# Kernel optimization log

Measured on AMD Instinct MI355X. Metric: run time of the kernel, lower is better.

## Reference

```python
import jax, jax.numpy as jnp
import numpy as np

NEG_SLOPE = 0.01  # nn.LeakyReLU default


def gcn_conv(x, src, dst, deg_inv_sqrt, W, b, n_nodes):
    """PyG GCNConv with self-loops already folded into (src, dst, deg_inv_sqrt).
    out = scatter_add(norm_e * (x @ W)[src]) + b, norm_e = d_src^-1/2 * d_dst^-1/2."""
    h = x @ W  # [N, F_out] -- transform first (F_out < F_in saves gather traffic)
    norm = (deg_inv_sqrt[src] * deg_inv_sqrt[dst])[:, None]  # [E, 1]
    msg = h[src] * norm  # [E, F_out]
    return jax.ops.segment_sum(msg, dst, num_segments=n_nodes) + b


def setup_inputs() -> dict:
    key = jax.random.key(0)
    ks = jax.random.split(key, 8)
    N, E, F_IN, F_HID, F_OUT = 50000, 800000, 256, 128, 64
    x = jax.random.normal(ks[0], (N, F_IN), dtype=jnp.float32)
    edge_index = jax.random.randint(ks[1], (2, E), 0, N, dtype=jnp.int64)
    def glorot(k, shape):
        lim = float(np.sqrt(6.0 / (shape[0] + shape[1])))
        return jax.random.uniform(k, shape, jnp.float32, -lim, lim)
    return {
        "x": x,
        "edge_index": edge_index,
        "W1": glorot(ks[2], (F_IN, F_HID)),
        "b1": jnp.zeros((F_HID,), jnp.float32),
        "W_mu": glorot(ks[3], (F_HID, F_OUT)),
        "b_mu": jnp.zeros((F_OUT,), jnp.float32),
        "W_logvar": glorot(ks[4], (F_HID, F_OUT)),
        "b_logvar": jnp.zeros((F_OUT,), jnp.float32),
    }


def reference(x, edge_index, W1, b1, W_mu, b_mu, W_logvar, b_logvar):
    n_nodes = x.shape[0]
    loops = jnp.arange(n_nodes, dtype=edge_index.dtype)
    src = jnp.concatenate([edge_index[0], loops])
    dst = jnp.concatenate([edge_index[1], loops])
    # degree on destination nodes (includes self-loop); >= 1 so rsqrt is safe
    deg = jax.ops.segment_sum(jnp.ones_like(dst, dtype=x.dtype), dst, num_segments=n_nodes)
    deg_inv_sqrt = jax.lax.rsqrt(deg)

    h = gcn_conv(x, src, dst, deg_inv_sqrt, W1, b1, n_nodes)
    h = jax.nn.leaky_relu(h, NEG_SLOPE)
    mu = gcn_conv(h, src, dst, deg_inv_sqrt, W_mu, b_mu, n_nodes)
    logvar = gcn_conv(h, src, dst, deg_inv_sqrt, W_logvar, b_logvar, n_nodes)
    return (mu, logvar)
```

## Files before the change

kernel.cpp:

```cpp
#include <hip/hip_runtime.h>

#define NEG_SLOPE 0.01f
#define EPB 4096
#define NB_SHIFT 8

typedef __attribute__((ext_vector_type(8))) short bf16x8;
typedef __attribute__((ext_vector_type(4))) float floatx4;

__device__ __forceinline__ short f2bf(float f) {
    union { float f; unsigned u; } v; v.f = f;
    unsigned u = v.u;
    u += 0x7FFF + ((u >> 16) & 1);
    return (short)(u >> 16);
}
__device__ __forceinline__ float bf2f(short s) {
    union { unsigned u; float f; } v;
    v.u = ((unsigned)(unsigned short)s) << 16;
    return v.f;
}

__launch_bounds__(256)
__global__ void hist_pack(const int* __restrict__ dst, int E, int B, int K,
                          int* __restrict__ btot,
                          const float* __restrict__ W1, const float* __restrict__ Wmu,
                          const float* __restrict__ Wlv,
                          short* __restrict__ w1f, short* __restrict__ wcatf) {
    __shared__ int lh[256];
    int bid = blockIdx.x;
    int tid = threadIdx.x;
    if (bid < B) {
        lh[tid] = 0;
        __syncthreads();
        int lo = bid * EPB, hi = min(lo + EPB, E);
        for (int e = lo + tid; e < hi; e += 256)
            atomicAdd(&lh[dst[e] >> NB_SHIFT], 1);
        __syncthreads();
        int v = lh[tid];
        if (v) atomicAdd(&btot[tid], v);
    } else {
        int i = (bid - B) * 256 + tid;
        if (i < 128 * 256) {
            int j  = i & 7;
            int ln = (i >> 3) & 15;
            int q  = (i >> 7) & 3;
            int t  = (i >> 9) & 7;
            int kb = i >> 12;
            int n = t * 16 + ln;
            int k = kb * 32 + q * 8 + j;
            w1f[i] = f2bf(W1[k * 128 + n]);
        } else {
            int i2 = i - 128 * 256;
            int j  = i2 & 7;
            int ln = (i2 >> 3) & 15;
            int q  = (i2 >> 7) & 3;
            int t  = (i2 >> 9) & 7;
            int kb = i2 >> 12;
            int n = t * 16 + ln;
            int k = kb * 32 + q * 8 + j;
            wcatf[i2] = f2bf((n < 64) ? Wmu[k * 64 + n] : Wlv[k * 64 + (n - 64)]);
        }
    }
}

__global__ void bucket_scan(const int* __restrict__ btot, int K, int E,
                            int* __restrict__ bstart, int* __restrict__ bcur) {
    __shared__ int waveTot[4];
    __shared__ int waveOff[4];
    int tid = threadIdx.x;
    int lane = tid & 63, wave = tid >> 6;
    int v = (tid < K) ? btot[tid] : 0;
    int s = v;
    #pragma unroll
    for (int o = 1; o < 64; o <<= 1) {
        int t = __shfl_up(s, o);
        if (lane >= o) s += t;
    }
    if (lane == 63) waveTot[wave] = s;
    __syncthreads();
    if (tid == 0) {
        int acc = 0;
        #pragma unroll
        for (int w = 0; w < 4; w++) { waveOff[w] = acc; acc += waveTot[w]; }
    }
    __syncthreads();
    int excl = s - v + waveOff[wave];
    if (tid < K) { bstart[tid] = excl; bcur[tid] = excl; }
    if (tid == 0) bstart[K] = E;
}

template<int K>
__device__ __forceinline__ void gemm1_body(int blk, int tid, const float* __restrict__ Ap,
                                           const short* __restrict__ Bfrag,
                                           short* __restrict__ C, int M) {
    int w = tid >> 6;
    int lane = tid & 63;
    int ln = lane & 15;
    int q  = lane >> 4;
    int rowTile = blk * 128 + w * 32;

    int r0 = rowTile + ln;
    int r1 = rowTile + 16 + ln;
    int r0c = (r0 < M) ? r0 : (M - 1);
    int r1c = (r1 < M) ? r1 : (M - 1);

    const float* a0F = Ap + (size_t)r0c * K + q * 8;
    const float* a1F = Ap + (size_t)r1c * K + q * 8;
    const short* bLane = Bfrag + lane * 8;

    floatx4 acc[2][8];
    #pragma unroll
    for (int f = 0; f < 2; f++)
        #pragma unroll
        for (int t = 0; t < 8; t++) acc[f][t] = (floatx4){0.f, 0.f, 0.f, 0.f};

    constexpr int NIT = K / 32;
    #pragma unroll
    for (int kb = 0; kb < NIT; kb++) {
        int kt = kb * 32;
        bf16x8 aF0, aF1;
        float4 x0 = *(const float4*)(a0F + kt);
        float4 x1 = *(const float4*)(a0F + kt + 4);
        float4 y0 = *(const float4*)(a1F + kt);
        float4 y1 = *(const float4*)(a1F + kt + 4);
        aF0[0] = f2bf(x0.x); aF0[1] = f2bf(x0.y); aF0[2] = f2bf(x0.z); aF0[3] = f2bf(x0.w);
        aF0[4] = f2bf(x1.x); aF0[5] = f2bf(x1.y); aF0[6] = f2bf(x1.z); aF0[7] = f2bf(x1.w);
        aF1[0] = f2bf(y0.x); aF1[1] = f2bf(y0.y); aF1[2] = f2bf(y0.z); aF1[3] = f2bf(y0.w);
        aF1[4] = f2bf(y1.x); aF1[5] = f2bf(y1.y); aF1[6] = f2bf(y1.z); aF1[7] = f2bf(y1.w);
        bf16x8 bF[8];
        #pragma unroll
        for (int t = 0; t < 8; t++)
            bF[t] = *(const bf16x8*)(bLane + (size_t)(kb * 8 + t) * 512);
        #pragma unroll
        for (int t = 0; t < 8; t++) {
            acc[0][t] = __builtin_amdgcn_mfma_f32_16x16x32_bf16(aF0, bF[t], acc[0][t], 0, 0, 0);
            acc[1][t] = __builtin_amdgcn_mfma_f32_16x16x32_bf16(aF1, bF[t], acc[1][t], 0, 0, 0);
        }
    }

    #pragma unroll
    for (int f = 0; f < 2; f++) {
        #pragma unroll
        for (int reg = 0; reg < 4; reg++) {
            int r = rowTile + f * 16 + q * 4 + reg;
            if (r < M) {
                #pragma unroll
                for (int t = 0; t < 8; t++)
                    C[(size_t)r * 128 + t * 16 + ln] = f2bf(acc[f][t][reg]);
            }
        }
    }
}

__launch_bounds__(256)
__global__ void scatter_gemm1(const int* __restrict__ src, const int* __restrict__ dst,
                              int E, int B, int* __restrict__ bcur,
                              unsigned* __restrict__ bucketed,
                              const float* __restrict__ x, const short* __restrict__ w1f,
                              short* __restrict__ z1, int M) {
    __shared__ int lh[256];
    __shared__ int lofs[256];
    __shared__ int gbase[256];
    __shared__ unsigned srt[EPB];
    __shared__ int waveTot[4];
    __shared__ int waveOff[4];
    int bid = blockIdx.x;
    int tid = threadIdx.x;
    if (bid < B) {
        lh[tid] = 0;
        __syncthreads();
        int lo = bid * EPB, hi = min(lo + EPB, E);
        for (int e = lo + tid; e < hi; e += 256)
            atomicAdd(&lh[dst[e] >> NB_SHIFT], 1);
        __syncthreads();
        int v = lh[tid];
        int lane = tid & 63, wave = tid >> 6;
        int s = v;
        #pragma unroll
        for (int o = 1; o < 64; o <<= 1) {
            int t = __shfl_up(s, o);
            if (lane >= o) s += t;
        }
        if (lane == 63) waveTot[wave] = s;
        __syncthreads();
        if (tid == 0) {
            int acc = 0;
            #pragma unroll
            for (int w = 0; w < 4; w++) { waveOff[w] = acc; acc += waveTot[w]; }
        }
        __syncthreads();
        int excl = s - v + waveOff[wave];
        lofs[tid] = excl;
        if (v) gbase[tid] = atomicAdd(&bcur[tid], v);
        __syncthreads();
        lh[tid] = excl;
        __syncthreads();
        for (int e = lo + tid; e < hi; e += 256) {
            int d = dst[e];
            unsigned rec = (unsigned)(src[e] & 0xFFFF) | ((unsigned)d << 16);
            int p = atomicAdd(&lh[d >> NB_SHIFT], 1);
            srt[p] = rec;
        }
        __syncthreads();
        int cnt = hi - lo;
        for (int p = tid; p < cnt; p += 256) {
            unsigned r = srt[p];
            int k = r >> 24;
            bucketed[gbase[k] + (p - lofs[k])] = r;
        }
    } else {
        gemm1_body<256>(bid - B, tid, x, w1f, z1, M);
    }
}

__global__ void fill_csr_deg(const unsigned* __restrict__ bucketed,
                             const int* __restrict__ bstart,
                             int* __restrict__ row_ptr, int* __restrict__ row_end,
                             float* __restrict__ dis,
                             unsigned short* __restrict__ csr_src, int N) {
    __shared__ int cnt[256];
    __shared__ int rp[256];
    __shared__ int waveTot[4];
    __shared__ int waveOff[4];
    __shared__ unsigned short lcsr[8192];
    int k = blockIdx.x;
    int tid = threadIdx.x;
    int base = k << NB_SHIFT;
    cnt[tid] = 0;
    __syncthreads();
    int lo = bstart[k], hi = bstart[k + 1];
    int m = hi - lo;
    for (int e = lo + tid; e < hi; e += 256)
        atomicAdd(&cnt[(bucketed[e] >> 16) & 255], 1);
    __syncthreads();
    int v = cnt[tid];
    int lane = tid & 63, wave = tid >> 6;
    int s = v;
    #pragma unroll
    for (int o = 1; o < 64; o <<= 1) {
        int t = __shfl_up(s, o);
        if (lane >= o) s += t;
    }
    if (lane == 63) waveTot[wave] = s;
    __syncthreads();
    if (tid == 0) {
        int acc = 0;
        #pragma unroll
        for (int w = 0; w < 4; w++) { waveOff[w] = acc; acc += waveTot[w]; }
    }
    __syncthreads();
    int excl = s - v + waveOff[wave];
    rp[tid] = excl;
    int node = base + tid;
    if (node < N) {
        row_ptr[node] = lo + excl;
        row_end[node] = lo + excl + v;
        dis[node] = rsqrtf(1.0f + (float)v);
    }
    __syncthreads();
    if (m <= 8192) {
        for (int e = lo + tid; e < hi; e += 256) {
            unsigned sd = bucketed[e];
            int p = atomicAdd(&rp[(sd >> 16) & 255], 1);
            lcsr[p] = (unsigned short)(sd & 0xFFFFu);
        }
        __syncthreads();
        for (int i = tid; i < m; i += 256) csr_src[lo + i] = lcsr[i];
    } else {
        for (int e = lo + tid; e < hi; e += 256) {
            unsigned sd = bucketed[e];
            int p = atomicAdd(&rp[(sd >> 16) & 255], 1);
            csr_src[lo + p] = (unsigned short)(sd & 0xFFFFu);
        }
    }
}


__launch_bounds__(256)
__global__ void agg1_gemm2(const short* __restrict__ z1, const int* __restrict__ row_ptr,
                           const int* __restrict__ row_end,
                           const unsigned short* __restrict__ csr_src,
                           const float* __restrict__ dis, const float* __restrict__ b1,
                           const short* __restrict__ wcatf,
                           short* __restrict__ z2, int N) {
    __shared__ short htile[16 * 128];
    int tid = threadIdx.x;
    int w = tid >> 6;
    int lane = tid & 63;
    int qi = lane >> 4;
    int fl = lane & 15;
    int fo = fl * 8;
    int base = blockIdx.x * 16;

    const short* zb = z1 + fo;
    #pragma unroll 1
    for (int i = 0; i < 4; ++i) {
        int local = w * 4 + i;
        int node = base + local;
        int swz = ((local & 7) * 8);
        short* hrow = &htile[(local * 128 + fo) ^ swz];
        if (node < N) {
            int start = row_ptr[node], end = row_end[node];
            float acc[8];
            #pragma unroll
            for (int t = 0; t < 8; t++) acc[t] = 0.f;
            for (int bse = start; bse < end; bse += 64) {
                int n = end - bse; n = (n > 64) ? 64 : n;
                int idx = (int)csr_src[bse + ((lane < n) ? lane : 0)];
                float dl = dis[idx];
                for (int j = 0; j < n; j += 8) {
                    int j0 = j + qi;
                    int j1 = j0 + 4;
                    int c0 = (j0 < n) ? j0 : 0;
                    int c1 = (j1 < n) ? j1 : 0;
                    int s0 = __shfl(idx, c0);
                    int s1 = __shfl(idx, c1);
                    float d0 = __shfl(dl, c0);
                    float d1 = __shfl(dl, c1);
                    if (j0 >= n) d0 = 0.f;
                    if (j1 >= n) d1 = 0.f;
                    bf16x8 zv0 = *(const bf16x8*)(zb + (size_t)s0 * 128);
                    bf16x8 zv1 = *(const bf16x8*)(zb + (size_t)s1 * 128);
                    #pragma unroll
                    for (int t = 0; t < 8; t++)
                        acc[t] = fmaf(d0, bf2f(zv0[t]), fmaf(d1, bf2f(zv1[t]), acc[t]));
                }
            }
            if (qi == 0) {
                float dn = dis[node];
                bf16x8 zs = *(const bf16x8*)(zb + (size_t)node * 128);
                #pragma unroll
                for (int t = 0; t < 8; t++) acc[t] = fmaf(dn, bf2f(zs[t]), acc[t]);
            }
            #pragma unroll
            for (int t = 0; t < 8; t++) {
                acc[t] += __shfl_xor(acc[t], 16);
                acc[t] += __shfl_xor(acc[t], 32);
            }
            if (qi == 0) {
                float d = dis[node];
                bf16x8 ov;
                #pragma unroll
                for (int t = 0; t < 8; t++) {
                    float v = fmaf(d, acc[t], b1[fo + t]);
                    v = (v > 0.f) ? v : NEG_SLOPE * v;
                    ov[t] = f2bf(v);
                }
                *(bf16x8*)hrow = ov;
            }
        } else if (qi == 0) {
            *(bf16x8*)hrow = (bf16x8){0, 0, 0, 0, 0, 0, 0, 0};
        }
    }
    __syncthreads();

    int r0 = fl;
    const short* bLane = wcatf + lane * 8;

    floatx4 acc[2];
    #pragma unroll
    for (int t = 0; t < 2; t++) acc[t] = (floatx4){0.f, 0.f, 0.f, 0.f};

    #pragma unroll
    for (int kb = 0; kb < 4; kb++) {
        int k0 = kb * 32 + qi * 8;
        bf16x8 aF = *(const bf16x8*)&htile[(r0 * 128 + k0) ^ ((r0 & 7) * 8)];
        #pragma unroll
        for (int t = 0; t < 2; t++) {
            int tt = w * 2 + t;
            bf16x8 bF = *(const bf16x8*)(bLane + (size_t)(kb * 8 + tt) * 512);
            acc[t] = __builtin_amdgcn_mfma_f32_16x16x32_bf16(aF, bF, acc[t], 0, 0, 0);
        }
    }

    #pragma unroll
    for (int reg = 0; reg < 4; reg++) {
        int gr = base + qi * 4 + reg;
        if (gr < N) {
            float s = dis[gr];
            #pragma unroll
            for (int t = 0; t < 2; t++)
                z2[(size_t)gr * 128 + (w * 2 + t) * 16 + fl] = f2bf(s * acc[t][reg]);
        }
    }
}

__launch_bounds__(256)
__global__ void agg_layer2(const short* __restrict__ zp, const int* __restrict__ row_ptr,
                           const int* __restrict__ row_end,
                           const unsigned short* __restrict__ csr_src,
                           const float* __restrict__ dis, const float* __restrict__ b_mu,
                           const float* __restrict__ b_lv, float* __restrict__ out, int N) {
    int wave = threadIdx.x >> 6;
    int node = blockIdx.x * 4 + wave;
    if (node >= N) return;
    int lane = threadIdx.x & 63;
    int qi = lane >> 4;
    int fl = lane & 15;
    int fo = fl * 8;
    const short* zb = zp + fo;
    int start = row_ptr[node], end = row_end[node];
    float acc[8];
    #pragma unroll
    for (int t = 0; t < 8; t++) acc[t] = 0.f;
    for (int bse = start; bse < end; bse += 64) {
        int n = end - bse; n = (n > 64) ? 64 : n;
        int idx = (int)csr_src[bse + ((lane < n) ? lane : 0)];
        for (int j = 0; j < n; j += 8) {
            int j0 = j + qi;
            int j1 = j0 + 4;
            int c0 = (j0 < n) ? j0 : 0;
            int c1 = (j1 < n) ? j1 : 0;
            int s0 = __shfl(idx, c0);
            int s1 = __shfl(idx, c1);
            float w0 = (j0 < n) ? 1.f : 0.f;
            float w1 = (j1 < n) ? 1.f : 0.f;
            bf16x8 z0 = *(const bf16x8*)(zb + (size_t)s0 * 128);
            bf16x8 zv1 = *(const bf16x8*)(zb + (size_t)s1 * 128);
            #pragma unroll
            for (int t = 0; t < 8; t++)
                acc[t] = fmaf(w0, bf2f(z0[t]), fmaf(w1, bf2f(zv1[t]), acc[t]));
        }
    }
    if (qi == 0) {
        bf16x8 zs = *(const bf16x8*)(zb + (size_t)node * 128);
        #pragma unroll
        for (int t = 0; t < 8; t++) acc[t] += bf2f(zs[t]);
    }
    #pragma unroll
    for (int t = 0; t < 8; t++) {
        acc[t] += __shfl_xor(acc[t], 16);
        acc[t] += __shfl_xor(acc[t], 32);
    }
    if (qi == 0) {
        float d = dis[node];
        float r[8];
        if (fl < 8) {
            #pragma unroll
            for (int t = 0; t < 8; t++) r[t] = fmaf(d, acc[t], b_mu[fo + t]);
            float* p = out + (size_t)node * 64 + fo;
            *(float4*)p       = make_float4(r[0], r[1], r[2], r[3]);
            *(float4*)(p + 4) = make_float4(r[4], r[5], r[6], r[7]);
        } else {
            #pragma unroll
            for (int t = 0; t < 8; t++) r[t] = fmaf(d, acc[t], b_lv[fo - 64 + t]);
            float* p = out + (size_t)N * 64 + (size_t)node * 64 + (fo - 64);
            *(float4*)p       = make_float4(r[0], r[1], r[2], r[3]);
            *(float4*)(p + 4) = make_float4(r[4], r[5], r[6], r[7]);
        }
    }
}


extern "C" void kernel_launch(void* const* d_in, const int* in_sizes, int n_in,
                              void* d_out, int out_size, void* d_ws, size_t ws_size,
                              hipStream_t stream) {
    const float* x   = (const float*)d_in[0];
    const int*   ei  = (const int*)d_in[1];
    const float* W1  = (const float*)d_in[2];
    const float* b1  = (const float*)d_in[3];
    const float* Wmu = (const float*)d_in[4];
    const float* bmu = (const float*)d_in[5];
    const float* Wlv = (const float*)d_in[6];
    const float* blv = (const float*)d_in[7];
    float* out = (float*)d_out;

    const int F_IN = 256;
    int N = in_sizes[0] / F_IN;
    int E = in_sizes[1] / 2;
    const int* e_src = ei;
    const int* e_dst = ei + E;

    int B = (E + EPB - 1) / EPB;
    int K = (N + 255) >> NB_SHIFT;
    int Ggemm = (N + 127) / 128;
    int G2 = (N + 15) / 16;

    char* ws = (char*)d_ws;
    size_t off = 0;
    auto carve = [&](size_t bytes) -> void* {
        void* p = ws + off;
        off += (bytes + 255) & ~(size_t)255;
        return p;
    };
    int*      row_end  = (int*)   carve((size_t)N * 4);
    int*      row_ptr  = (int*)   carve((size_t)N * 4);
    float*    dis      = (float*) carve((size_t)N * 4);
    unsigned short* csr_src = (unsigned short*)carve((size_t)E * 2);
    short*    bufA     = (short*) carve((size_t)N * 128 * 2);
    short*    bufB     = (short*) carve((size_t)N * 128 * 2);
    short*    w1f      = (short*) carve(128 * 256 * 2);
    short*    wcatf    = (short*) carve(128 * 128 * 2);
    int*      bstart   = (int*)   carve((size_t)(K + 1) * 4);
    int*      bcur     = (int*)   carve((size_t)K * 4);
    int*      btot     = (int*)   carve((size_t)K * 4);
    unsigned* bucketed = (unsigned*)carve((size_t)E * 4);

    hipMemsetAsync(btot, 0, (size_t)K * 4, stream);
    hipLaunchKernelGGL(hist_pack, dim3(B + 192), dim3(256), 0, stream,
                       e_dst, E, B, K, btot, W1, Wmu, Wlv, w1f, wcatf);
    hipLaunchKernelGGL(bucket_scan, dim3(1), dim3(256), 0, stream, btot, K, E, bstart, bcur);
    hipLaunchKernelGGL(scatter_gemm1, dim3(B + Ggemm), dim3(256), 0, stream,
                       e_src, e_dst, E, B, bcur, bucketed, x, w1f, bufA, N);
    hipLaunchKernelGGL(fill_csr_deg, dim3(K), dim3(256), 0, stream,
                       bucketed, bstart, row_ptr, row_end, dis, csr_src, N);
    hipLaunchKernelGGL(agg1_gemm2, dim3(G2), dim3(256), 0, stream,
                       bufA, row_ptr, row_end, csr_src, dis, b1, wcatf, bufB, N);
    hipLaunchKernelGGL(agg_layer2, dim3((N + 3) / 4), dim3(256), 0, stream,
                       bufB, row_ptr, row_end, csr_src, dis, bmu, blv, out, N);
}
```

Measured before the change: 212.9 us.

## Assign one node per quarter-wave in both aggregation kernels

Both aggregation kernels now map each 16-lane quarter of a wave to its own node instead of spreading one node's edges across the whole wave. This removes the cross-quarter shuffle reductions and idle lanes when degree is low (average about 17), and lets four nodes' gathers be in flight per wave. Per-quarter loops now diverge when neighbouring nodes have different degrees, and each quarter walks its edge list serially in groups of 4. The agg_layer2 grid shrinks to G2 blocks of 16 nodes each.

New measurement: 204.6 us. -3.9%, faster.

```diff
diff --git a/kernel.cpp b/kernel.cpp
--- a/kernel.cpp
+++ b/kernel.cpp
@@ -275,6 +275,36 @@
 }
 
 
+template<bool WEIGHTED>
+__device__ __forceinline__ void agg_quarter(const short* __restrict__ zb,
+                                            const unsigned short* __restrict__ csr_src,
+                                            const float* __restrict__ dis,
+                                            int start, int end, int qbase, int fl,
+                                            float acc[8]) {
+    for (int bse = start; bse < end; bse += 16) {
+        int n = end - bse; n = (n > 16) ? 16 : n;
+        int idx = (int)csr_src[bse + ((fl < n) ? fl : 0)];
+        float dl = WEIGHTED ? dis[idx] : 1.f;
+        for (int e = 0; e < 16; e += 4) {
+            if (e >= n) break;
+            #pragma unroll
+            for (int k = 0; k < 4; ++k) {
+                int ee = e + k;
+                int s0 = __shfl(idx, qbase + ee);
+                float we;
+                if (WEIGHTED) we = __shfl(dl, qbase + ee);
+                else          we = 1.f;
+                if (ee >= n) we = 0.f;
+                bf16x8 zv = *(const bf16x8*)(zb + (size_t)s0 * 128);
+                #pragma unroll
+                for (int t = 0; t < 8; t++)
+                    acc[t] = fmaf(we, bf2f(zv[t]), acc[t]);
+            }
+        }
+    }
+}
+
+
 __launch_bounds__(256)
 __global__ void agg1_gemm2(const short* __restrict__ z1, const int* __restrict__ row_ptr,
                            const int* __restrict__ row_end,
@@ -289,68 +319,32 @@
     int qi = lane >> 4;
     int fl = lane & 15;
     int fo = fl * 8;
+    int qbase = qi * 16;
     int base = blockIdx.x * 16;
-
-    const short* zb = z1 + fo;
-    #pragma unroll 1
-    for (int i = 0; i < 4; ++i) {
-        int local = w * 4 + i;
-        int node = base + local;
-        int swz = ((local & 7) * 8);
-        short* hrow = &htile[(local * 128 + fo) ^ swz];
-        if (node < N) {
-            int start = row_ptr[node], end = row_end[node];
-            float acc[8];
-            #pragma unroll
-            for (int t = 0; t < 8; t++) acc[t] = 0.f;
-            for (int bse = start; bse < end; bse += 64) {
-                int n = end - bse; n = (n > 64) ? 64 : n;
-                int idx = (int)csr_src[bse + ((lane < n) ? lane : 0)];
-                float dl = dis[idx];
-                for (int j = 0; j < n; j += 8) {
-                    int j0 = j + qi;
-                    int j1 = j0 + 4;
-                    int c0 = (j0 < n) ? j0 : 0;
-                    int c1 = (j1 < n) ? j1 : 0;
-                    int s0 = __shfl(idx, c0);
-                    int s1 = __shfl(idx, c1);
-                    float d0 = __shfl(dl, c0);
-                    float d1 = __shfl(dl, c1);
-                    if (j0 >= n) d0 = 0.f;
-                    if (j1 >= n) d1 = 0.f;
-                    bf16x8 zv0 = *(const bf16x8*)(zb + (size_t)s0 * 128);
-                    bf16x8 zv1 = *(const bf16x8*)(zb + (size_t)s1 * 128);
-                    #pragma unroll
-                    for (int t = 0; t < 8; t++)
-                        acc[t] = fmaf(d0, bf2f(zv0[t]), fmaf(d1, bf2f(zv1[t]), acc[t]));
-                }
-            }
-            if (qi == 0) {
-                float dn = dis[node];
-                bf16x8 zs = *(const bf16x8*)(zb + (size_t)node * 128);
-                #pragma unroll
-                for (int t = 0; t < 8; t++) acc[t] = fmaf(dn, bf2f(zs[t]), acc[t]);
-            }
-            #pragma unroll
-            for (int t = 0; t < 8; t++) {
-                acc[t] += __shfl_xor(acc[t], 16);
-                acc[t] += __shfl_xor(acc[t], 32);
-            }
-            if (qi == 0) {
-                float d = dis[node];
-                bf16x8 ov;
-                #pragma unroll
-                for (int t = 0; t < 8; t++) {
-                    float v = fmaf(d, acc[t], b1[fo + t]);
-                    v = (v > 0.f) ? v : NEG_SLOPE * v;
-                    ov[t] = f2bf(v);
-                }
-                *(bf16x8*)hrow = ov;
-            }
-        } else if (qi == 0) {
-            *(bf16x8*)hrow = (bf16x8){0, 0, 0, 0, 0, 0, 0, 0};
-        }
-    }
+    int local = w * 4 + qi;
+    int node = base + local;
+
+    short* hrow = &htile[(local * 128 + fo) ^ ((local & 7) * 8)];
+    bf16x8 ov = (bf16x8){0, 0, 0, 0, 0, 0, 0, 0};
+    if (node < N) {
+        const short* zb = z1 + fo;
+        int start = row_ptr[node], end = row_end[node];
+        float acc[8];
+        #pragma unroll
+        for (int t = 0; t < 8; t++) acc[t] = 0.f;
+        agg_quarter<true>(zb, csr_src, dis, start, end, qbase, fl, acc);
+        float dn = dis[node];
+        bf16x8 zs = *(const bf16x8*)(zb + (size_t)node * 128);
+        #pragma unroll
+        for (int t = 0; t < 8; t++) acc[t] = fmaf(dn, bf2f(zs[t]), acc[t]);
+        #pragma unroll
+        for (int t = 0; t < 8; t++) {
+            float v = fmaf(dn, acc[t], b1[fo + t]);
+            v = (v > 0.f) ? v : NEG_SLOPE * v;
+            ov[t] = f2bf(v);
+        }
+    }
+    *(bf16x8*)hrow = ov;
     __syncthreads();
 
     int r0 = fl;
@@ -390,63 +384,40 @@
                            const unsigned short* __restrict__ csr_src,
                            const float* __restrict__ dis, const float* __restrict__ b_mu,
                            const float* __restrict__ b_lv, float* __restrict__ out, int N) {
-    int wave = threadIdx.x >> 6;
-    int node = blockIdx.x * 4 + wave;
-    if (node >= N) return;
-    int lane = threadIdx.x & 63;
+    int tid = threadIdx.x;
+    int w = tid >> 6;
+    int lane = tid & 63;
     int qi = lane >> 4;
     int fl = lane & 15;
     int fo = fl * 8;
+    int qbase = qi * 16;
+    int node = blockIdx.x * 16 + w * 4 + qi;
+    if (node >= N) return;
+
     const short* zb = zp + fo;
     int start = row_ptr[node], end = row_end[node];
     float acc[8];
     #pragma unroll
     for (int t = 0; t < 8; t++) acc[t] = 0.f;
-    for (int bse = start; bse < end; bse += 64) {
-        int n = end - bse; n = (n > 64) ? 64 : n;
-        int idx = (int)csr_src[bse + ((lane < n) ? lane : 0)];
-        for (int j = 0; j < n; j += 8) {
-            int j0 = j + qi;
-            int j1 = j0 + 4;
-            int c0 = (j0 < n) ? j0 : 0;
-            int c1 = (j1 < n) ? j1 : 0;
-            int s0 = __shfl(idx, c0);
-            int s1 = __shfl(idx, c1);
-            float w0 = (j0 < n) ? 1.f : 0.f;
-            float w1 = (j1 < n) ? 1.f : 0.f;
-            bf16x8 z0 = *(const bf16x8*)(zb + (size_t)s0 * 128);
-            bf16x8 zv1 = *(const bf16x8*)(zb + (size_t)s1 * 128);
-            #pragma unroll
-            for (int t = 0; t < 8; t++)
-                acc[t] = fmaf(w0, bf2f(z0[t]), fmaf(w1, bf2f(zv1[t]), acc[t]));
-        }
-    }
-    if (qi == 0) {
-        bf16x8 zs = *(const bf16x8*)(zb + (size_t)node * 128);
-        #pragma unroll
-        for (int t = 0; t < 8; t++) acc[t] += bf2f(zs[t]);
-    }
-    #pragma unroll
-    for (int t = 0; t < 8; t++) {
-        acc[t] += __shfl_xor(acc[t], 16);
-        acc[t] += __shfl_xor(acc[t], 32);
-    }
-    if (qi == 0) {
-        float d = dis[node];
-        float r[8];
-        if (fl < 8) {
-            #pragma unroll
-            for (int t = 0; t < 8; t++) r[t] = fmaf(d, acc[t], b_mu[fo + t]);
-            float* p = out + (size_t)node * 64 + fo;
-            *(float4*)p       = make_float4(r[0], r[1], r[2], r[3]);
-            *(float4*)(p + 4) = make_float4(r[4], r[5], r[6], r[7]);
-        } else {
-            #pragma unroll
-            for (int t = 0; t < 8; t++) r[t] = fmaf(d, acc[t], b_lv[fo - 64 + t]);
-            float* p = out + (size_t)N * 64 + (size_t)node * 64 + (fo - 64);
-            *(float4*)p       = make_float4(r[0], r[1], r[2], r[3]);
-            *(float4*)(p + 4) = make_float4(r[4], r[5], r[6], r[7]);
-        }
+    agg_quarter<false>(zb, csr_src, nullptr, start, end, qbase, fl, acc);
+    bf16x8 zs = *(const bf16x8*)(zb + (size_t)node * 128);
+    #pragma unroll
+    for (int t = 0; t < 8; t++) acc[t] += bf2f(zs[t]);
+
+    float d = dis[node];
+    float r[8];
+    if (fl < 8) {
+        #pragma unroll
+        for (int t = 0; t < 8; t++) r[t] = fmaf(d, acc[t], b_mu[fo + t]);
+        float* p = out + (size_t)node * 64 + fo;
+        *(float4*)p       = make_float4(r[0], r[1], r[2], r[3]);
+        *(float4*)(p + 4) = make_float4(r[4], r[5], r[6], r[7]);
+    } else {
+        #pragma unroll
+        for (int t = 0; t < 8; t++) r[t] = fmaf(d, acc[t], b_lv[fo - 64 + t]);
+        float* p = out + (size_t)N * 64 + (size_t)node * 64 + (fo - 64);
+        *(float4*)p       = make_float4(r[0], r[1], r[2], r[3]);
+        *(float4*)(p + 4) = make_float4(r[4], r[5], r[6], r[7]);
     }
 }
 
@@ -505,6 +476,6 @@
                        bucketed, bstart, row_ptr, row_end, dis, csr_src, N);
     hipLaunchKernelGGL(agg1_gemm2, dim3(G2), dim3(256), 0, stream,
                        bufA, row_ptr, row_end, csr_src, dis, b1, wcatf, bufB, N);
-    hipLaunchKernelGGL(agg_layer2, dim3((N + 3) / 4), dim3(256), 0, stream,
+    hipLaunchKernelGGL(agg_layer2, dim3(G2), dim3(256), 0, stream,
                        bufB, row_ptr, row_end, csr_src, dis, bmu, blv, out, N);
 }
```
